# Kernel optimization log

Measured on AMD Instinct MI355X. Metric: run time of the kernel, lower is better.

## Reference

```python
import jax, jax.numpy as jnp
import numpy as np
from math import factorial

# ---- static sizes from S2ConvNet_original ----
B_IN, B1, B2 = 30, 10, 6   # bandwidths: input S2 grid, after conv1 (SO3), after conv2 (SO3)
F1, F2, FOUT = 20, 40, 10
BATCH = 128


def _wigner_d(l, beta):
    """Wigner small-d matrix d^l_{m',m}(beta); rows m'=-l..l, cols m=-l..l."""
    cb, sb = np.cos(beta / 2.0), np.sin(beta / 2.0)
    d = np.zeros((2 * l + 1, 2 * l + 1))
    for i, mp in enumerate(range(-l, l + 1)):
        for j, m in enumerate(range(-l, l + 1)):
            pref = np.sqrt(float(factorial(l + mp) * factorial(l - mp) * factorial(l + m) * factorial(l - m)))
            acc = 0.0
            for s in range(max(0, m - mp), min(l + m, l - mp) + 1):
                den = factorial(l + m - s) * factorial(s) * factorial(mp - m + s) * factorial(l - mp - s)
                acc += ((-1.0) ** (mp - m + s) / den) * cb ** (2 * l + m - mp - 2 * s) * sb ** (mp - m + 2 * s)
            d[i, j] = pref * acc
    return d


def _dh_quad(b):
    """Driscoll-Healy beta grid / weights: sum_j w_j g(beta_j) ~ int_0^pi g(b) sin(b) db."""
    j = np.arange(2 * b)
    beta = np.pi * (2 * j + 1) / (4 * b)
    k = np.arange(b)[:, None]
    w = (2.0 / b) * np.sin(beta) * np.sum(np.sin((2 * k + 1) * beta[None, :]) / (2 * k + 1), axis=0)
    return beta, w


def _s2_grid(max_beta=np.pi / 8, n_alpha=8, n_beta=3):
    beta = np.arange(1, n_beta + 1) * max_beta / n_beta
    alpha = np.linspace(0, 2 * np.pi, n_alpha, endpoint=False)
    Bm, Am = np.meshgrid(beta, alpha, indexing='ij')
    return np.stack([Bm.ravel(), Am.ravel()], 1)  # [24, 2]


def _so3_grid(max_beta=np.pi / 8, max_gamma=2 * np.pi, n_alpha=8, n_beta=3, n_gamma=8):
    beta = np.arange(1, n_beta + 1) * max_beta / n_beta
    alpha = np.linspace(0, 2 * np.pi, n_alpha, endpoint=False)
    pre_gamma = np.linspace(0, max_gamma, n_gamma, endpoint=False)
    Bm, Am, Cm = np.meshgrid(beta, alpha, pre_gamma, indexing='ij')
    return np.stack([Bm.ravel(), Am.ravel(), (Cm - Am).ravel()], 1)  # [192, 3]


# ---------- conv1: S2 analysis (b 30 -> 10) ----------
_beta30, _qw30 = _dh_quad(B_IN)
_A1 = np.concatenate(
    [np.stack([_wigner_d(l, bb)[:, l] for bb in _beta30])  # d^l_{m,0}(beta_j): [60, 2l+1]
     * (_qw30 * (2 * np.pi / (2 * B_IN)))[:, None]
     for l in range(B1)], axis=1)  # [60, 100]
_A1J = jnp.asarray(_A1.astype(np.float32))
_M1 = np.concatenate([np.arange(-l, l + 1) for l in range(B1)])
_M1_IDX = np.mod(_M1, 2 * B_IN)

_g1 = _s2_grid()
_Y1 = np.concatenate(
    [np.stack([_wigner_d(l, bb)[:, l] for bb in _g1[:, 0]])
     * np.exp(-1j * np.outer(_g1[:, 1], np.arange(-l, l + 1)))
     for l in range(B1)], axis=1)  # [24, 100] complex
_Y1J = jnp.asarray(_Y1.astype(np.complex64))
_SC1 = float(1.0 / np.sqrt(len(_g1) * 1 * (B1 ** 4) / (B_IN ** 2)))

# ---------- SO3 synthesis tables at b=10 ----------
_beta10, _qw10 = _dh_quad(B1)
_D1S = [jnp.asarray(((2 * l + 1) * np.stack([_wigner_d(l, bb) for bb in _beta10])).astype(np.float32)) for l in range(B1)]
_FM1 = [np.mod(np.arange(-l, l + 1), 2 * B1) for l in range(B1)]

# ---------- conv2: SO3 analysis (b 10 -> 6) ----------
_W3 = np.concatenate(
    [(np.stack([_wigner_d(l, bb) for bb in _beta10])  # [20, 2l+1, 2l+1]
      * (_qw10 * (2 * np.pi / (2 * B1)) ** 2)[:, None, None]).reshape(2 * B1, -1)
     for l in range(B2)], axis=1)  # [20, 286]
_W3J = jnp.asarray(_W3.astype(np.float32))
_M2 = np.concatenate([np.repeat(np.arange(-l, l + 1), 2 * l + 1) for l in range(B2)])
_N2 = np.concatenate([np.tile(np.arange(-l, l + 1), 2 * l + 1) for l in range(B2)])
_M2_IDX = np.mod(_M2, 2 * B1)
_N2_IDX = np.mod(_N2, 2 * B1)

_g2 = _so3_grid()
_Y2 = np.concatenate(
    [np.stack([_wigner_d(l, bb) for bb in _g2[:, 0]]).reshape(len(_g2), -1)
     * (np.exp(-1j * np.outer(_g2[:, 1], np.arange(-l, l + 1)))[:, :, None]
        * np.exp(-1j * np.outer(_g2[:, 2], np.arange(-l, l + 1)))[:, None, :]).reshape(len(_g2), -1)
     for l in range(B2)], axis=1)  # [192, 286] complex: D^l_{mn}(alpha,beta,gamma)
_Y2J = jnp.asarray(_Y2.astype(np.complex64))
_SC2 = float(1.0 / np.sqrt(len(_g2) * F1 * (B2 ** 3) / (B1 ** 3)))

# ---------- SO3 synthesis tables at b=6 + integration weights ----------
_beta6, _qw6 = _dh_quad(B2)
_D2S = [jnp.asarray(((2 * l + 1) * np.stack([_wigner_d(l, bb) for bb in _beta6])).astype(np.float32)) for l in range(B2)]
_FM2 = [np.mod(np.arange(-l, l + 1), 2 * B2) for l in range(B2)]
_W_INT = jnp.asarray((_qw6 * (2 * np.pi / (2 * B2)) ** 2).astype(np.float32))


def _forward(x, k1, bias1, k2, bias2, w_out, b_lin):
    Bn = x.shape[0]
    # ===== conv1: S2 correlation -> function on SO(3) at b=10 =====
    xf = jnp.fft.fft(x.astype(jnp.complex64), axis=-1)                 # FFT over alpha: [B,1,60,60]
    xhat = jnp.einsum('bfjs,js->sbf', xf[..., _M1_IDX], _A1J)          # [100,B,1] S2 spectrum
    k1h = jnp.einsum('iop,ps->sio', (k1 * _SC1).astype(jnp.complex64), _Y1J)  # [100,1,F1]
    Ffreq = jnp.zeros((Bn, F1, 2 * B1, 2 * B1, 2 * B1), jnp.complex64)  # [B,F1,beta,m,n]
    for l in range(B1):
        s0, s1 = l * l, (l + 1) * (l + 1)
        # z^l_{mn} = sum_fin xhat^l_m conj(khat^l_n)  (outer product per degree l)
        zl = jnp.einsum('mbi,nio->bmno', xhat[s0:s1], jnp.conj(k1h[s0:s1]))
        fb = jnp.einsum('bmno,jmn->bojmn', zl, _D1S[l])                # (2l+1) d^l_{mn}(beta_j)
        Ffreq = Ffreq.at[:, :, :, _FM1[l][:, None], _FM1[l][None, :]].add(fb)
    x1 = jnp.fft.ifft2(Ffreq, axes=(-2, -1)).real * float((2 * B1) ** 2)  # synth over alpha,gamma
    x1 = jax.nn.relu(x1 + bias1[None, :, None, None, None])            # [B,F1,20,20,20]
    # ===== conv2: SO(3) correlation -> b=6 =====
    x1f = jnp.fft.fft2(x1.astype(jnp.complex64), axes=(-2, -1))        # FFT over alpha,gamma
    xhat2 = jnp.einsum('bfjs,js->sbf', x1f[:, :, :, _M2_IDX, _N2_IDX], _W3J)  # [286,B,F1]
    k2h = jnp.einsum('iop,ps->sio', (k2 * _SC2).astype(jnp.complex64), _Y2J)  # [286,F1,F2]
    Ffreq2 = jnp.zeros((Bn, F2, 2 * B2, 2 * B2, 2 * B2), jnp.complex64)
    base = 0
    for l in range(B2):
        L = 2 * l + 1
        xl = xhat2[base:base + L * L].reshape(L, L, Bn, F1)            # [m,k,B,Fin]
        gl = jnp.conj(k2h[base:base + L * L].reshape(L, L, F1, F2))    # [n,k,Fin,Fout]
        zl = jnp.einsum('mkbi,nkio->bmno', xl, gl)                     # z^l = xhat^l ghat^l^H
        fb = jnp.einsum('bmno,jmn->bojmn', zl, _D2S[l])
        Ffreq2 = Ffreq2.at[:, :, :, _FM2[l][:, None], _FM2[l][None, :]].add(fb)
        base += L * L
    x2 = jnp.fft.ifft2(Ffreq2, axes=(-2, -1)).real * float((2 * B2) ** 2)
    x2 = jax.nn.relu(x2 + bias2[None, :, None, None, None])            # [B,F2,12,12,12]
    # ===== so3_integrate + linear head =====
    feat = jnp.einsum('bfjkp,j->bf', x2, _W_INT)                       # [B,F2]
    return feat @ w_out.T + b_lin


def setup_inputs() -> dict:
    key = jax.random.key(0)
    ks = jax.random.split(key, 4)
    return {
        'x': jax.random.normal(ks[0], (BATCH, 1, 2 * B_IN, 2 * B_IN), jnp.float32),
        'k1': jax.random.normal(ks[1], (1, F1, len(_g1)), jnp.float32),
        'bias1': jnp.zeros((F1,), jnp.float32),
        'k2': jax.random.normal(ks[2], (F1, F2, len(_g2)), jnp.float32),
        'bias2': jnp.zeros((F2,), jnp.float32),
        'w_out': jax.random.normal(ks[3], (FOUT, F2), jnp.float32) / np.sqrt(F2).astype(np.float32),
        'b_lin': jnp.zeros((FOUT,), jnp.float32),
    }


def reference(x, k1, bias1, k2, bias2, w_out, b_lin):
    return _forward(x, k1, bias1, k2, bias2, w_out, b_lin)
```

## Files before the change

### kernel.cpp

```cpp
#include <hip/hip_runtime.h>
#include <math.h>

#define PI_D 3.14159265358979323846

#define BATCH 128
#define F1 20
#define F2 40
#define FOUT 10
#define NS1 100
#define NS2 286
#define NH2 146

typedef float v2f __attribute__((ext_vector_type(2)));
#define PKFMA(a,b,c) __builtin_elementwise_fma((a),(b),(c))
#define SW(v) __builtin_shufflevector((v),(v),1,0)
static __device__ __forceinline__ v2f bc2(float s){ return (v2f){s,s}; }
static __device__ __forceinline__ v2f ldv(const float2* p){ return *(const v2f*)p; }

#define GLOAD_LDS16(g,l) __builtin_amdgcn_global_load_lds( \
  (const __attribute__((address_space(1))) void*)(g), \
  (__attribute__((address_space(3))) void*)(l), 16, 0, 0)

__constant__ int ZB10c[11] = {0,1,10,35,84,165,286,455,680,969,1330};
__constant__ int B2OFFc[7] = {0,1,10,35,84,165,286};
__constant__ int HOFFc[7]  = {0,1,6,19,44,85,146};
__constant__ float2 E8c[8] = {
  { 1.f, 0.f}, { 0.70710678118654752f,-0.70710678118654752f},
  { 0.f,-1.f}, {-0.70710678118654752f,-0.70710678118654752f},
  {-1.f, 0.f}, {-0.70710678118654752f, 0.70710678118654752f},
  { 0.f, 1.f}, { 0.70710678118654752f, 0.70710678118654752f}};

#define WFENCE do{ __builtin_amdgcn_sched_barrier(0); \
  asm volatile("s_waitcnt lgkmcnt(0)" ::: "memory"); \
  __builtin_amdgcn_sched_barrier(0); }while(0)

__device__ inline void h_decode(int h, int& l, int& m, int& n){
  l=0; while(HOFFc[l+1]<=h) ++l;
  int r=h-HOFFc[l], L=2*l+1;
  if(r<l+1){ n=0; m=r; }
  else { int q=r-(l+1); n=q/L+1; m=q%L-l; }
}

__device__ inline double ipow_d(double x, int n){ double r=1.0; for(int i=0;i<n;++i) r*=x; return r; }

__device__ double wigd_t(int l, int mp, int m, double beta, const double* F){
  double cb=cos(0.5*beta), sb=sin(0.5*beta);
  double pref=sqrt(F[l+mp]*F[l-mp]*F[l+m]*F[l-m]);
  int s0 = (m-mp>0) ? (m-mp) : 0;
  int s1 = (l+m < l-mp) ? (l+m) : (l-mp);
  double acc=0.0;
  for(int s=s0;s<=s1;++s){
    double den=F[l+m-s]*F[s]*F[mp-m+s]*F[l-mp-s];
    double t=ipow_d(cb,2*l+m-mp-2*s)*ipow_d(sb,mp-m+2*s)/den;
    acc += ((mp-m+s)&1)? -t : t;
  }
  return pref*acc;
}

__device__ double dhw(int b, int j){
  double beta=PI_D*(2*j+1)/(4.0*b);
  double s=0.0;
  for(int k=0;k<b;++k) s += sin((2*k+1)*beta)/(2*k+1);
  return (2.0/b)*sin(beta)*s;
}

__global__ void gen_all(const float* __restrict__ k2,
                        float* A1, float* D1SJ, float* W3H, float* D2SJ,
                        float* D3_2, float* D3_1, float* WINT,
                        float2* E60, float2* E20, float2* E12,
                        unsigned* zLUT, unsigned* xh2LUT, unsigned* h2LUT,
                        unsigned short* fhLUT, unsigned* aLUT,
                        float2* KA){
  __shared__ double factS[21];
  __shared__ double dhwS[60];
  __shared__ float2 E8L[8];
  int blk=blockIdx.x, t=threadIdx.x;
  if(t==0){ double f=1.0; factS[0]=1.0; for(int k=1;k<=20;++k){ f*=(double)k; factS[k]=f; } }
  if(blk<24){ if(t<60) dhwS[t]=dhw(30,t); }
  else if(blk>=76 && blk<82){ if(t<20) dhwS[t]=dhw(10,t); }
  if(t<8) E8L[t]=E8c[t];
  __syncthreads();
  const double* F=factS;
  if(blk<24){
    int idx=blk*256+t;
    if(idx<6000){
      int j=idx/NS1, s=idx%NS1;
      int l=0; while((l+1)*(l+1)<=s) ++l;
      int m=s-l*l-l;
      double beta=PI_D*(2*j+1)/120.0;
      A1[idx]=(float)(wigd_t(l,m,0,beta,F)*dhwS[j]*(2.0*PI_D/60.0));
    }
  } else if(blk<76){
    int idx=(blk-24)*256+t; if(idx>=13300) return;
    int j=idx/1330, s=idx%1330;
    int l=0; while(ZB10c[l+1]<=s) ++l;
    int r=s-ZB10c[l]; int L=2*l+1;
    int mi=r/L, ni=r%L;
    double beta=PI_D*(2*j+1)/40.0;
    float v=(float)((2*l+1)*wigd_t(l,mi-l,ni-l,beta,F));
    D1SJ[j*1330+s]=v;
    int s2=ZB10c[l]+(2*l-mi)*L+ni;
    D1SJ[(19-j)*1330+s2]=(ni&1)? -v : v;
  } else if(blk<82){
    int idx=(blk-76)*256+t;
    if(idx<10*NH2){
      int j=idx/NH2, h=idx%NH2;
      int l,m,n; h_decode(h,l,m,n);
      double beta=PI_D*(2*j+1)/40.0;
      double c=2.0*PI_D/20.0;
      float v=(float)(wigd_t(l,m,n,beta,F)*dhwS[j]*c*c);
      W3H[j*NH2+h]=v;
      if(n==0){
        W3H[(19-j)*NH2+h]=((l+m)&1)? -v : v;
      } else {
        int L=2*l+1;
        int hp=HOFFc[l]+(l+1)+(n-1)*L+(l-m);
        W3H[(19-j)*NH2+hp]=((l+n)&1)? -v : v;
      }
    }
  } else if(blk<89){
    int idx=(blk-82)*256+t; if(idx>=1716) return;
    int j=idx/286, s=idx%286;
    int l=0; while(B2OFFc[l+1]<=s) ++l;
    int r=s-B2OFFc[l]; int L=2*l+1;
    int mi=r/L, ni=r%L;
    double beta=PI_D*(2*j+1)/24.0;
    float v=(float)((2*l+1)*wigd_t(l,mi-l,ni-l,beta,F));
    D2SJ[j*286+s]=v;
    int s2=B2OFFc[l]+(2*l-mi)*L+ni;
    D2SJ[(11-j)*286+s2]=(ni&1)? -v : v;
  } else if(blk<93){
    int idx=(blk-89)*256+t; if(idx>=3*286) return;
    int bi=idx/286, s=idx%286;
    int l=0; while(B2OFFc[l+1]<=s) ++l;
    int r=s-B2OFFc[l]; int L=2*l+1;
    int mi=r/L, ni=r%L;
    double beta=(bi+1)*(PI_D/8.0)/3.0;
    D3_2[idx]=(float)wigd_t(l,mi-l,ni-l,beta,F);
  } else if(blk<95){
    int idx=(blk-93)*256+t; if(idx>=3*100) return;
    int bi=idx/100, s=idx%100;
    int l=0; while((l+1)*(l+1)<=s) ++l;
    int m=s-l*l-l;
    double beta=(bi+1)*(PI_D/8.0)/3.0;
    D3_1[idx]=(float)wigd_t(l,m,0,beta,F);
  } else if(blk==95){
    if(t<12){ double c=2.0*PI_D/12.0; WINT[t]=(float)(dhw(6,t)*c*c); }
    if(t<60){ double a=2.0*PI_D*t/60.0; E60[t]=make_float2((float)cos(a),(float)sin(a)); }
    if(t<20){ double a=2.0*PI_D*t/20.0; E20[t]=make_float2((float)cos(a),(float)sin(a)); }
    if(t<12){ double a=2.0*PI_D*t/12.0; E12[t]=make_float2((float)cos(a),(float)sin(a)); }
  } else if(blk<102){
    int idx=(blk-96)*256+t; if(idx>=1330) return;
    int l=0; while(ZB10c[l+1]<=idx) ++l;
    int r=idx-ZB10c[l], L=2*l+1;
    int mi=r/L, ni=r%L;
    unsigned s1x=(unsigned)(l*l+mi), s1k=(unsigned)(l*l+ni);
    zLUT[idx]=s1x|(s1k<<16);
  } else if(blk==102){
    if(t<146){
      int l,m,n; h_decode(t,l,m,n);
      int L=2*l+1;
      int s2 =B2OFFc[l]+(m+l)*L+(n+l);
      int s2p=B2OFFc[l]+(l-m)*L+(l-n);
      unsigned sg=(unsigned)((m+n)&1);
      xh2LUT[t]=(unsigned)s2 | ((unsigned)s2p<<10) | (sg<<20);
      h2LUT[t]=(unsigned)l | ((unsigned)(m+l)<<4) | ((unsigned)(n+l)<<8) | ((unsigned)s2<<12);
      fhLUT[t]=(unsigned short)((n==0)? m : 6+(n-1)*11+(m+5));
    }
  } else if(blk==103){
    if(t==0){
      int idx=0;
      for(int lm=0;lm<10;++lm){
        for(int m=0;m<10;++m){
          int nlo=(m==0)?0:-9;
          for(int n=nlo;n<10;++n){
            int an=n<0?-n:n;
            int lmin=m>an?m:an;
            if(lmin!=lm) continue;
            int L=2*lm+1;
            int zi=ZB10c[lm]+(m+lm)*L+(n+lm);
            aLUT[idx++]=(unsigned)zi | ((unsigned)m<<11) | ((unsigned)(n+9)<<15) | ((unsigned)lm<<20);
          }
        }
      }
    }
  } else {
    int idx=(blk-104)*256+t;
    if(idx<153600){
      int ai=idx&7, q=(idx>>3)&7;
      int r2=idx>>6;
      int bi=r2%3, io=r2/3;
      const float* kp=k2+(size_t)io*192+bi*64+ai*8;
      v2f acc={0.f,0.f};
      int ph=0;
      #pragma unroll
      for(int gi=0;gi<8;++gi){
        acc=PKFMA(bc2(kp[gi]), ldv(&E8L[ph]), acc);
        ph=(ph+q)&7;
      }
      KA[(size_t)io*192+bi*64+q*8+ai]=make_float2(acc.x,acc.y);
    }
  }
}

__global__ __launch_bounds__(256) void front_k(const float* __restrict__ x,
    const float* __restrict__ k1,
    const float2* __restrict__ E60, const float* __restrict__ A1,
    const float* __restrict__ D3_1,
    float2* __restrict__ XHAT, float2* __restrict__ K1H){
  int blk=blockIdx.x, t=threadIdx.x;
  if(blk<128){
    __shared__ __align__(16) float xs[3600];
    __shared__ float2 E60s[60];
    __shared__ float2 XFs[1140];
    if(t<60){ float2 e=E60[t]; E60s[t]=make_float2(e.x,-e.y); }
    {
      const float4* src=(const float4*)(x+blk*3600);
      float4* dst=(float4*)xs;
      for(int i=t;i<900;i+=256) GLOAD_LDS16(src+i, dst+(i&~63));
    }
    __syncthreads();
    for(int idx=t; idx<1140; idx+=256){
      int j=idx/19, mi=idx%19;
      int step=(mi<9)? mi+51 : mi-9;
      bool modd = ((mi&1)==0);
      const float* xr=xs+j*60;
      v2f acc={0.f,0.f};
      int k=0;
      for(int a=0;a<30;++a){
        float xv = modd ? (xr[a]-xr[a+30]) : (xr[a]+xr[a+30]);
        acc=PKFMA(bc2(xv), ldv(&E60s[k]), acc);
        k+=step; if(k>=60)k-=60;
      }
      XFs[idx]=make_float2(acc.x,acc.y);
    }
    __syncthreads();
    for(int s=t; s<100; s+=256){
      int l=0; while((l+1)*(l+1)<=s) ++l;
      int m=s-l*l-l;
      const float2* xf=&XFs[m+9];
      v2f acc={0.f,0.f};
      for(int j=0;j<60;++j){
        acc=PKFMA(bc2(A1[j*NS1+s]), ldv(&xf[j*19]), acc);
      }
      XHAT[blk*NS1+s]=make_float2(acc.x,acc.y);
    }
  } else {
    __shared__ float2 E8s[8];
    if(t<8) E8s[t]=E8c[t];
    __syncthreads();
    int idx=(blk-128)*256+t;
    if(idx<F1*NS1){
      int o=idx/NS1, s=idx%NS1;
      int l=0; while((l+1)*(l+1)<=s) ++l;
      int m=s-l*l-l;
      int mm=m&7;
      v2f acc={0.f,0.f};
      for(int bi=0;bi<3;++bi){
        v2f sum={0.f,0.f};
        int q=0;
        #pragma unroll
        for(int ai=0;ai<8;++ai){
          sum=PKFMA(bc2(k1[o*24+bi*8+ai]), ldv(&E8s[q]), sum);
          q=(q+mm)&7;
        }
        acc=PKFMA(bc2(D3_1[bi*100+s]), sum, acc);
      }
      const float SC1f = 0.06123724356957945f;
      K1H[idx]=make_float2(acc.x*SC1f, acc.y*SC1f);
    }
  }
}

__global__ __launch_bounds__(512,6) void fused1(
    const float2* __restrict__ XHAT, const float2* __restrict__ K1H,
    const float* __restrict__ D1SJ, const float* __restrict__ W3H,
    const float2* __restrict__ E20, const float* __restrict__ bias1,
    const unsigned* __restrict__ zLUT, const unsigned* __restrict__ xh2LUT,
    const unsigned short* __restrict__ fhLUT, const unsigned* __restrict__ aLUT,
    float2* __restrict__ XH2){
  const int b=blockIdx.x, o=blockIdx.y, t=threadIdx.x;
  const int ln=t&63, w=t>>6;
  __shared__ __align__(16) float2 zS[1330];
  __shared__ __align__(16) float2 TWE2[400];
  __shared__ __align__(16) float2 regA[8][200];
  __shared__ __align__(16) float2 regB[8][190];

  for(int idx=t; idx<400; idx+=512){
    int r=idx/20, c=idx%20;
    TWE2[idx]=E20[(r*c)%20];
  }
  {
    float2* st=regA[0];
    if(t<100) st[t]=XHAT[b*NS1+t];
    else if(t<200) st[t]=K1H[o*NS1+(t-100)];
  }
  __syncthreads();
  {
    const float2* st=regA[0];
    for(int idx=t; idx<1330; idx+=512){
      unsigned u=zLUT[idx];
      v2f xa=ldv(&st[u&0xffff]);
      v2f kb=ldv(&st[100+(u>>16)]);
      v2f p1=xa*kb, p2=xa*SW(kb);
      zS[idx]=make_float2(p1.x+p1.y, p2.y-p2.x);
    }
  }
  __syncthreads();

  const float bb1=bias1[o];
  float2* G  = regA[w];
  float*  vbF= (float*)regA[w];
  float2* Fq = regA[w];
  float*  RB = (float*)regB[w];
  float*  Sx = RB;
  float*  Sy = RB+180;
  float*  T0f= RB+360;
  float2* U_T= regB[w];
  v2f fa0={0.f,0.f}, fa1=fa0, fa2=fa0;

  const int BROW[19]={11,12,13,14,15,16,17,18,19,0,1,2,3,4,5,6,7,8,9};

  for(int jq=0;jq<3;++jq){
    const int j=jq*8+w;
    const bool act=(j<20);
    const float* Dg=D1SJ + (act? j*1330 : 0);
    if(act) for(int idx=ln; idx<181; idx+=64){
      unsigned au=aLUT[idx];
      int zi=au&2047;
      int m=(au>>11)&15, n9=(au>>15)&31, l=(au>>20)&15;
      int L=2*l+1;
      int m2=2*m+2;
      v2f a0={0.f,0.f};
      for(; l<10; ++l){
        a0=PKFMA(ldv(&zS[zi]), bc2(Dg[zi]), a0);
        zi += L*L + 2*L + m2; L += 2;
      }
      *(v2f*)&G[m*19+n9]=a0;
    }
    WFENCE;
    if(act){
    if(ln<45){
      int mb=ln/5+1, gp=(ln%5)*2;
      const float2* Gr=&G[mb*19];
      v2f E1a={0.f,0.f},E2a=E1a,O1a=E1a,O2a=E1a;
      v2f E1b=E1a,E2b=E1a,O1b=E1a,O2b=E1a;
      #pragma unroll
      for(int c=0;c<19;++c){
        v2f gv=ldv(&Gr[c]);
        const float* er=(const float*)&TWE2[BROW[c]*20+gp];
        float4 e01=*(const float4*)er;
        v2f e0={e01.x,e01.y}, e1={e01.z,e01.w};
        if(c&1){
          E1a=PKFMA(gv,e0,E1a); E2a=PKFMA(gv,SW(e0),E2a);
          E1b=PKFMA(gv,e1,E1b); E2b=PKFMA(gv,SW(e1),E2b);
        } else {
          O1a=PKFMA(gv,e0,O1a); O2a=PKFMA(gv,SW(e0),O2a);
          O1b=PKFMA(gv,e1,O1b); O2b=PKFMA(gv,SW(e1),O2b);
        }
      }
      int si=(mb-1)*20+gp;
      float exa=E1a.x-E1a.y, oxa=O1a.x-O1a.y;
      float eya=E2a.x+E2a.y, oya=O2a.x+O2a.y;
      float exb=E1b.x-E1b.y, oxb=O1b.x-O1b.y;
      float eyb=E2b.x+E2b.y, oyb=O2b.x+O2b.y;
      *(v2f*)&Sx[si]   =(v2f){2.f*(exa+oxa), 2.f*(exb+oxb)};
      *(v2f*)&Sx[si+10]=(v2f){2.f*(exa-oxa), 2.f*(exb-oxb)};
      *(v2f*)&Sy[si]   =(v2f){2.f*(eya+oya), 2.f*(eyb+oyb)};
      *(v2f*)&Sy[si+10]=(v2f){2.f*(eya-oya), 2.f*(eyb-oyb)};
    } else if(ln<50){
      int gt=(ln-45)*2;
      float g0x=G[9].x;
      float Ea=0.f,Eb=0.f,Oa=0.f,Ob=0.f;
      #pragma unroll
      for(int n=1;n<10;++n){
        float2 gv=G[9+n];
        const float* er=(const float*)&TWE2[n*20+gt];
        float4 e01=*(const float4*)er;
        float ra=gv.x*e01.x-gv.y*e01.y;
        float rb=gv.x*e01.z-gv.y*e01.w;
        if((n&1)==0){ Ea+=ra; Eb+=rb; } else { Oa+=ra; Ob+=rb; }
      }
      T0f[gt]   =g0x+2.f*(Ea+Oa);
      T0f[gt+1] =g0x+2.f*(Eb+Ob);
      T0f[gt+10]=g0x+2.f*(Ea-Oa);
      T0f[gt+11]=g0x+2.f*(Eb-Ob);
    }
    }
    WFENCE;
    if(act && ln<50){
      int a=ln/5, g0=(ln%5)*4;
      v2f i01={T0f[g0]+bb1, T0f[g0+1]+bb1};
      v2f i23={T0f[g0+2]+bb1, T0f[g0+3]+bb1};
      v2f P01={0.f,0.f},P23=P01,Q01=P01,Q23=P01;
      #pragma unroll
      for(int m=1;m<10;++m){
        float2 e=TWE2[a*20+m];
        v2f sx01=*(const v2f*)&Sx[(m-1)*20+g0];
        v2f sx23=*(const v2f*)&Sx[(m-1)*20+g0+2];
        v2f sy01=*(const v2f*)&Sy[(m-1)*20+g0];
        v2f sy23=*(const v2f*)&Sy[(m-1)*20+g0+2];
        if(m&1){
          Q01=PKFMA(bc2(e.x),sx01,Q01); Q01=PKFMA(bc2(-e.y),sy01,Q01);
          Q23=PKFMA(bc2(e.x),sx23,Q23); Q23=PKFMA(bc2(-e.y),sy23,Q23);
        } else {
          P01=PKFMA(bc2(e.x),sx01,P01); P01=PKFMA(bc2(-e.y),sy01,P01);
          P23=PKFMA(bc2(e.x),sx23,P23); P23=PKFMA(bc2(-e.y),sy23,P23);
        }
      }
      v2f z2={0.f,0.f};
      v2f vA01=i01+P01+Q01, vA23=i23+P23+Q23;
      v2f vB01=i01+P01-Q01, vB23=i23+P23-Q23;
      *(v2f*)&vbF[a*20+g0]       =__builtin_elementwise_max(vA01,z2);
      *(v2f*)&vbF[a*20+g0+2]     =__builtin_elementwise_max(vA23,z2);
      *(v2f*)&vbF[(a+10)*20+g0]  =__builtin_elementwise_max(vB01,z2);
      *(v2f*)&vbF[(a+10)*20+g0+2]=__builtin_elementwise_max(vB23,z2);
    }
    WFENCE;
    if(act && ln<60){
      int a=ln/3, np=ln%3;
      int nu0=2*np, nu1=2*np+1;
      int r0=(np==0)?0:(20-2*np);
      int r1=19-2*np;
      const float* vp=&vbF[a*20];
      const float2* T0r=&TWE2[r0*20];
      const float2* T1r=&TWE2[r1*20];
      v2f u0={0.f,0.f}, u1=u0;
      #pragma unroll
      for(int g=0;g<10;++g){
        float va=vp[g], vb=vp[g+10];
        u0=PKFMA(bc2(va+vb), ldv(&T0r[g]), u0);
        u1=PKFMA(bc2(va-vb), ldv(&T1r[g]), u1);
      }
      *(v2f*)&U_T[nu0*20+a]=u0; *(v2f*)&U_T[nu1*20+a]=u1;
    }
    WFENCE;
    if(act && ln<61){
      int mu,nu;
      if(ln<6){ mu=ln; nu=0; } else { int q=ln-6; nu=q/11+1; mu=q%11-5; }
      int mm=(mu+20)%20;
      int rm=(20-mm)%20;
      bool modd=(mm&1);
      const float2* Ur=&U_T[nu*20];
      const float2* Er=&TWE2[rm*20];
      v2f p1={0.f,0.f}, p2=p1;
      #pragma unroll
      for(int a=0;a<10;++a){
        v2f ua=ldv(&Ur[a]), ub=ldv(&Ur[a+10]);
        v2f u = modd ? (ua-ub) : (ua+ub);
        v2f e=ldv(&Er[a]);
        p1=PKFMA(u,e,p1);
        p2=PKFMA(u,SW(e),p2);
      }
      Fq[ln]=make_float2(p1.x-p1.y, p2.x+p2.y);
    }
    WFENCE;
    if(act){
      const float* W3r=W3H + j*NH2;
      fa0=PKFMA(bc2(W3r[ln]),    ldv(&Fq[fhLUT[ln]]),    fa0);
      fa1=PKFMA(bc2(W3r[64+ln]), ldv(&Fq[fhLUT[64+ln]]), fa1);
      if(ln<18) fa2=PKFMA(bc2(W3r[128+ln]), ldv(&Fq[fhLUT[128+ln]]), fa2);
    }
    WFENCE;
  }
  regB[w][ln]=make_float2(fa0.x,fa0.y);
  regB[w][64+ln]=make_float2(fa1.x,fa1.y);
  if(ln<18) regB[w][128+ln]=make_float2(fa2.x,fa2.y);
  __syncthreads();
  float2* XHrow=XH2+(size_t)(b*F1+o)*286;
  for(int h=t; h<146; h+=512){
    unsigned u=xh2LUT[h];
    int s2=u&1023, s2p=(u>>10)&1023;
    float sg=((u>>20)&1)? -1.f : 1.f;
    float2 a0=regB[0][h], a1=regB[1][h], a2=regB[2][h], a3=regB[3][h];
    float2 a4=regB[4][h], a5=regB[5][h], a6=regB[6][h], a7=regB[7][h];
    float2 a=make_float2(a0.x+a1.x+a2.x+a3.x+a4.x+a5.x+a6.x+a7.x,
                         a0.y+a1.y+a2.y+a3.y+a4.y+a5.y+a6.y+a7.y);
    XHrow[s2 ]=a;
    XHrow[s2p]=make_float2(sg*a.x, -sg*a.y);
  }
}

__global__ __launch_bounds__(192) void k2h_k(const float2* __restrict__ KA,
                      const float* __restrict__ D3_2,
                      const unsigned* __restrict__ h2LUT, const unsigned* __restrict__ xh2LUT,
                      float2* __restrict__ K2H){
  __shared__ float2 kaS[192];
  __shared__ float2 E8s[8];
  int io=blockIdx.x, t=threadIdx.x;
  int i=io/F2, o=io%F2;
  if(t<8) E8s[t]=E8c[t];
  kaS[t]=KA[(size_t)io*192+t];
  __syncthreads();
  if(t>=146) return;
  unsigned hu=h2LUT[t];
  int l=hu&15, mi=(hu>>4)&15, ni=(hu>>8)&15, s2=hu>>12;
  int m=mi-l, n=ni-l;
  unsigned xu=xh2LUT[t];
  int s2p=(xu>>10)&1023;
  float sg=((xu>>20)&1)? -1.f : 1.f;
  int q=n&7, p=(m-n)&7;
  v2f a1={0.f,0.f}, a2=a1;
  for(int bi=0;bi<3;++bi){
    const float2* kp=&kaS[bi*64+q*8];
    v2f s1={0.f,0.f}, s2v=s1;
    int ph=0;
    #pragma unroll
    for(int ai=0;ai<8;++ai){
      v2f ka=ldv(&kp[ai]), e=ldv(&E8s[ph]);
      s1=PKFMA(ka,e,s1); s2v=PKFMA(ka,SW(e),s2v);
      ph=(ph+p)&7;
    }
    v2f dv=bc2(D3_2[bi*286+s2]);
    a1=PKFMA(dv,s1,a1); a2=PKFMA(dv,s2v,a2);
  }
  const float SC2f = 0.034722222222222224f;
  float re=(a1.x-a1.y)*SC2f, im=(a2.x+a2.y)*SC2f;
  float2* Krow=K2H+(size_t)(o*F1+i)*286;
  Krow[s2 ]=make_float2(re,im);
  Krow[s2p]=make_float2(sg*re,-sg*im);
}

__global__ __launch_bounds__(256,3) void fused2(
    const float2* __restrict__ XH2, const float2* __restrict__ K2H,
    const float* __restrict__ D2SJ, const float* __restrict__ WINT,
    const float2* __restrict__ E12, const float* __restrict__ bias2,
    const unsigned* __restrict__ h2LUT, const unsigned* __restrict__ xh2LUT,
    float* __restrict__ FEAT){
  const int b=blockIdx.x, o=blockIdx.y, t=threadIdx.x;
  const int ln=t&63, w=t>>6;
  __shared__ __align__(16) float2 Xs[2541];
  __shared__ __align__(16) float2 Ks[2541];
  __shared__ float2 zpS[1144];
  __shared__ float2 z2S[286];
  __shared__ float  redS[256];
  float2* alias=(float2*)Xs;
  float2* TWE12=alias;

  const int gb[4]={0,84,165,286};
  const int hb[4]={0,44,85,146};
  for(int grp=0; grp<3; ++grp){
    int row0=gb[grp], rows=gb[grp+1]-row0;
    {
      int cnt=20*rows;
      const float2* xbase=XH2+(size_t)b*F1*286+row0;
      const float2* kbase=K2H+(size_t)o*F1*286+row0;
      for(int idx=t; idx<cnt; idx+=256){
        int i=idx/rows, sl=idx-i*rows;
        Xs[sl*21+i]=xbase[i*286+sl];
        Ks[sl*21+i]=kbase[i*286+sl];
      }
    }
    __syncthreads();
    int nh=hb[grp+1]-hb[grp];
    for(int idx=t; idx<4*nh; idx+=256){
      int hl=idx>>2, iq=idx&3;
      int h=hb[grp]+hl;
      unsigned hu=h2LUT[h];
      int l=hu&15, mi=(hu>>4)&15, ni=(hu>>8)&15, s2=hu>>12;
      int L=2*l+1;
      int xr0=(B2OFFc[l]-row0)+mi*L;
      int kr0=(B2OFFc[l]-row0)+ni*L;
      v2f p1={0.f,0.f}, p2=p1;
      for(int k=0;k<L;++k){
        const float2* xp=Xs+(xr0+k)*21+iq*5;
        const float2* kp=Ks+(kr0+k)*21+iq*5;
        #pragma unroll
        for(int i=0;i<5;++i){
          v2f xa=ldv(&xp[i]), kb=ldv(&kp[i]);
          p1=PKFMA(xa,kb,p1);
          p2=PKFMA(xa,SW(kb),p2);
        }
      }
      zpS[iq*286+s2]=make_float2(p1.x+p1.y, p2.y-p2.x);
    }
    __syncthreads();
  }
  for(int idx=t; idx<146; idx+=256){
    unsigned xu=xh2LUT[idx];
    int s2=xu&1023, s2p=(xu>>10)&1023;
    float sg=((xu>>20)&1)? -1.f : 1.f;
    float2 a;
    a.x=zpS[0*286+s2].x+zpS[1*286+s2].x+zpS[2*286+s2].x+zpS[3*286+s2].x;
    a.y=zpS[0*286+s2].y+zpS[1*286+s2].y+zpS[2*286+s2].y+zpS[3*286+s2].y;
    z2S[s2]=a;
    z2S[s2p]=make_float2(sg*a.x,-sg*a.y);
  }
  __syncthreads();
  for(int idx=t; idx<144; idx+=256){
    int r=idx/12, c=idx%12;
    TWE12[idx]=E12[(r*c)%12];
  }
  __syncthreads();

  float2* base2=alias+144+w*400;
  float2* G2_0=base2; float2* G2_1=base2+66; float2* G2_2=base2+132;
  float*  SP=(float*)(base2+198);
  float*  S2x0=SP, *S2x1=SP+60, *S2x2=SP+120;
  float*  S2y0=SP+180, *S2y1=SP+240, *S2y2=SP+300;
  float*  T02=SP+360;
  float personal=0.f;
  const float b2v=bias2[o];
  const int j0=3*w, j1=3*w+1, j2=3*w+2;
  const float* Dg0=D2SJ + j0*286;
  const float* Dg1=D2SJ + j1*286;
  const float* Dg2=D2SJ + j2*286;
  const int BR12[11]={7,8,9,10,11,0,1,2,3,4,5};

  if(ln<61){
    int m,n;
    if(ln<6){m=0;n=ln;} else {int qq=ln-6;m=qq/11+1;n=qq%11-5;}
    int an=n<0?-n:n; int l=m>an?m:an; int L=2*l+1;
    int zi=B2OFFc[l]+(m+l)*L+(n+l); int m2=2*m+2;
    v2f a0={0.f,0.f}, a1=a0, a2=a0;
    for(;l<6;++l){
      v2f zv=ldv(&z2S[zi]);
      a0=PKFMA(zv, bc2(Dg0[zi]), a0);
      a1=PKFMA(zv, bc2(Dg1[zi]), a1);
      a2=PKFMA(zv, bc2(Dg2[zi]), a2);
      zi+=L*L+2*L+m2; L+=2;
    }
    int gi=m*11+(n+5);
    *(v2f*)&G2_0[gi]=a0; *(v2f*)&G2_1[gi]=a1; *(v2f*)&G2_2[gi]=a2;
  }
  WFENCE;
  if(ln<30){
    int m=ln/6+1, g=ln%6;
    v2f E1_0={0.f,0.f},E2_0=E1_0,O1_0=E1_0,O2_0=E1_0;
    v2f E1_1=E1_0,E2_1=E1_0,O1_1=E1_0,O2_1=E1_0;
    v2f E1_2=E1_0,E2_2=E1_0,O1_2=E1_0,O2_2=E1_0;
    #pragma unroll
    for(int c=0;c<11;++c){
      float2 ef=TWE12[BR12[c]*12+g];
      v2f e={ef.x,ef.y};
      v2f g0=ldv(&G2_0[m*11+c]), g1=ldv(&G2_1[m*11+c]), g2=ldv(&G2_2[m*11+c]);
      if(c&1){
        E1_0=PKFMA(g0,e,E1_0); E2_0=PKFMA(g0,SW(e),E2_0);
        E1_1=PKFMA(g1,e,E1_1); E2_1=PKFMA(g1,SW(e),E2_1);
        E1_2=PKFMA(g2,e,E1_2); E2_2=PKFMA(g2,SW(e),E2_2);
      } else {
        O1_0=PKFMA(g0,e,O1_0); O2_0=PKFMA(g0,SW(e),O2_0);
        O1_1=PKFMA(g1,e,O1_1); O2_1=PKFMA(g1,SW(e),O2_1);
        O1_2=PKFMA(g2,e,O1_2); O2_2=PKFMA(g2,SW(e),O2_2);
      }
    }
    int si=(m-1)*12+g;
    {
      float Ex=E1_0.x-E1_0.y, Ox=O1_0.x-O1_0.y;
      float Ey=E2_0.x+E2_0.y, Oy=O2_0.x+O2_0.y;
      S2x0[si]=2.f*(Ex+Ox); S2x0[si+6]=2.f*(Ex-Ox);
      S2y0[si]=2.f*(Ey+Oy); S2y0[si+6]=2.f*(Ey-Oy);
    }
    {
      float Ex=E1_1.x-E1_1.y, Ox=O1_1.x-O1_1.y;
      float Ey=E2_1.x+E2_1.y, Oy=O2_1.x+O2_1.y;
      S2x1[si]=2.f*(Ex+Ox); S2x1[si+6]=2.f*(Ex-Ox);
      S2y1[si]=2.f*(Ey+Oy); S2y1[si+6]=2.f*(Ey-Oy);
    }
    {
      float Ex=E1_2.x-E1_2.y, Ox=O1_2.x-O1_2.y;
      float Ey=E2_2.x+E2_2.y, Oy=O2_2.x+O2_2.y;
      S2x2[si]=2.f*(Ex+Ox); S2x2[si+6]=2.f*(Ex-Ox);
      S2y2[si]=2.f*(Ey+Oy); S2y2[si+6]=2.f*(Ey-Oy);
    }
  } else if(ln<42){
    int g=ln-30;
    float r0=G2_0[5].x, r1=G2_1[5].x, r2=G2_2[5].x;
    #pragma unroll
    for(int n=1;n<6;++n){
      float2 e=TWE12[n*12+g];
      float2 g0=G2_0[5+n], g1=G2_1[5+n], g2=G2_2[5+n];
      r0+=2.f*(g0.x*e.x-g0.y*e.y);
      r1+=2.f*(g1.x*e.x-g1.y*e.y);
      r2+=2.f*(g2.x*e.x-g2.y*e.y);
    }
    T02[g]=r0; T02[12+g]=r1; T02[24+g]=r2;
  }
  WFENCE;
  if(ln<36){
    float w0=WINT[j0], w1=WINT[j1], w2=WINT[j2];
    int a=ln/3, g4=(ln%3)*4;
    v2f iA0={T02[g4]+b2v, T02[g4+1]+b2v},       iB0={T02[g4+2]+b2v, T02[g4+3]+b2v};
    v2f iA1={T02[12+g4]+b2v, T02[12+g4+1]+b2v}, iB1={T02[12+g4+2]+b2v, T02[12+g4+3]+b2v};
    v2f iA2={T02[24+g4]+b2v, T02[24+g4+1]+b2v}, iB2={T02[24+g4+2]+b2v, T02[24+g4+3]+b2v};
    #pragma unroll
    for(int m=1;m<6;++m){
      float2 e=TWE12[a*12+m];
      v2f ex=bc2(e.x), eny=bc2(-e.y);
      int si=(m-1)*12+g4;
      v2f sx, sy;
      sx=*(const v2f*)&S2x0[si];   sy=*(const v2f*)&S2y0[si];
      iA0=PKFMA(ex,sx,iA0); iA0=PKFMA(eny,sy,iA0);
      sx=*(const v2f*)&S2x0[si+2]; sy=*(const v2f*)&S2y0[si+2];
      iB0=PKFMA(ex,sx,iB0); iB0=PKFMA(eny,sy,iB0);
      sx=*(const v2f*)&S2x1[si];   sy=*(const v2f*)&S2y1[si];
      iA1=PKFMA(ex,sx,iA1); iA1=PKFMA(eny,sy,iA1);
      sx=*(const v2f*)&S2x1[si+2]; sy=*(const v2f*)&S2y1[si+2];
      iB1=PKFMA(ex,sx,iB1); iB1=PKFMA(eny,sy,iB1);
      sx=*(const v2f*)&S2x2[si];   sy=*(const v2f*)&S2y2[si];
      iA2=PKFMA(ex,sx,iA2); iA2=PKFMA(eny,sy,iA2);
      sx=*(const v2f*)&S2x2[si+2]; sy=*(const v2f*)&S2y2[si+2];
      iB2=PKFMA(ex,sx,iB2); iB2=PKFMA(eny,sy,iB2);
    }
    v2f z2={0.f,0.f};
    v2f rA0=__builtin_elementwise_max(iA0,z2), rB0=__builtin_elementwise_max(iB0,z2);
    v2f rA1=__builtin_elementwise_max(iA1,z2), rB1=__builtin_elementwise_max(iB1,z2);
    v2f rA2=__builtin_elementwise_max(iA2,z2), rB2=__builtin_elementwise_max(iB2,z2);
    personal += w0*(rA0.x+rA0.y+rB0.x+rB0.y)
              + w1*(rA1.x+rA1.y+rB1.x+rB1.y)
              + w2*(rA2.x+rA2.y+rB2.x+rB2.y);
  }
  redS[t]=personal;
  __syncthreads();
  for(int s=128;s>0;s>>=1){
    if(t<s) redS[t]+=redS[t+s];
    __syncthreads();
  }
  if(t==0) FEAT[b*F2+o]=redS[0];
}

__global__ void head_k(const float* __restrict__ FEAT, const float* __restrict__ w_out,
                       const float* __restrict__ b_lin, float* __restrict__ out){
  int idx=blockIdx.x*blockDim.x+threadIdx.x;
  if(idx>=BATCH*FOUT) return;
  int b=idx/FOUT, q=idx%FOUT;
  float acc=b_lin[q];
  for(int f=0;f<F2;++f) acc += FEAT[b*F2+f]*w_out[q*F2+f];
  out[idx]=acc;
}

extern "C" void kernel_launch(void* const* d_in, const int* in_sizes, int n_in,
                              void* d_out, int out_size, void* d_ws, size_t ws_size,
                              hipStream_t stream) {
  const float* x    =(const float*)d_in[0];
  const float* k1   =(const float*)d_in[1];
  const float* bias1=(const float*)d_in[2];
  const float* k2   =(const float*)d_in[3];
  const float* bias2=(const float*)d_in[4];
  const float* w_out=(const float*)d_in[5];
  const float* b_lin=(const float*)d_in[6];
  float* out=(float*)d_out;

  char* ws=(char*)d_ws;
  float*  A1   =(float* )(ws+0);
  float*  D1SJ =(float* )(ws+24000);
  float*  W3H  =(float* )(ws+130400);
  float*  D2SJ =(float* )(ws+142080);
  float*  D3_2 =(float* )(ws+155808);
  float*  D3_1 =(float* )(ws+159248);
  float*  WINT =(float* )(ws+160448);
  float2* E60  =(float2*)(ws+160496);
  float2* E20  =(float2*)(ws+160976);
  float2* E12  =(float2*)(ws+161136);
  unsigned* zLUT=(unsigned*)(ws+161248);
  unsigned* xh2LUT=(unsigned*)(ws+166576);
  unsigned* h2LUT =(unsigned*)(ws+167160);
  unsigned short* fhLUT=(unsigned short*)(ws+167744);
  unsigned* aLUT =(unsigned*)(ws+168048);
  float2* XHAT =(float2*)(ws+168784);
  float2* K1H  =(float2*)(ws+271184);
  float2* KA   =(float2*)(ws+287184);
  float2* XH2  =(float2*)(ws+1515984);
  float2* K2H  =(float2*)(ws+7373264);
  float*  FEAT =(float* )(ws+9203664);

  (void)in_sizes; (void)n_in; (void)out_size; (void)ws_size;

  gen_all<<<704,256,0,stream>>>(k2,A1,D1SJ,W3H,D2SJ,D3_2,D3_1,WINT,E60,E20,E12,
                                zLUT,xh2LUT,h2LUT,fhLUT,aLUT,KA);
  front_k<<<136,256,0,stream>>>(x,k1,E60,A1,D3_1,XHAT,K1H);
  dim3 g1(BATCH,F1);
  fused1<<<g1,512,0,stream>>>(XHAT,K1H,D1SJ,W3H,E20,bias1,zLUT,xh2LUT,fhLUT,aLUT,XH2);
  k2h_k<<<F1*F2,192,0,stream>>>(KA,D3_2,h2LUT,xh2LUT,K2H);
  dim3 g2(BATCH,F2);
  fused2<<<g2,256,0,stream>>>(XH2,K2H,D2SJ,WINT,E12,bias2,h2LUT,xh2LUT,FEAT);
  head_k<<<(BATCH*FOUT+255)/256,256,0,stream>>>(FEAT,w_out,b_lin,out);
}
```

Measured before the change: 237.2 us.

## Stage conv2 inputs with async global-to-LDS copies in two channel halves

The second-layer fused kernel no longer copies X and K spectra into shared memory with scalar, transposed stores across three row groups. It now copies contiguous halves of ten input channels with 16-byte global_load_lds transfers. In the compute loop each thread owns a full output coefficient and loops over ten channels in a channel-major layout. This cuts the staging passes from three to two, removes the per-element index arithmetic and makes the global reads coalesced. In exchange, only 146 of 256 threads work in the contraction phase, the padded layout that avoided bank conflicts is gone, and the reduction buffer now reuses zpS, which needs an extra barrier.

Result: no change. 241.4 us (+1.8%).

```diff
diff --git a/kernel.cpp b/kernel.cpp
--- a/kernel.cpp
+++ b/kernel.cpp
@@ -529,60 +529,52 @@
     float* __restrict__ FEAT){
   const int b=blockIdx.x, o=blockIdx.y, t=threadIdx.x;
   const int ln=t&63, w=t>>6;
-  __shared__ __align__(16) float2 Xs[2541];
-  __shared__ __align__(16) float2 Ks[2541];
-  __shared__ float2 zpS[1144];
+  __shared__ __align__(16) float2 Xs[2860];
+  __shared__ __align__(16) float2 Ks[2860];
+  __shared__ float2 zpS[572];
   __shared__ float2 z2S[286];
-  __shared__ float  redS[256];
+  float* redS=(float*)zpS;
   float2* alias=(float2*)Xs;
   float2* TWE12=alias;
 
-  const int gb[4]={0,84,165,286};
-  const int hb[4]={0,44,85,146};
-  for(int grp=0; grp<3; ++grp){
-    int row0=gb[grp], rows=gb[grp+1]-row0;
+  for(int hf=0; hf<2; ++hf){
     {
-      int cnt=20*rows;
-      const float2* xbase=XH2+(size_t)b*F1*286+row0;
-      const float2* kbase=K2H+(size_t)o*F1*286+row0;
-      for(int idx=t; idx<cnt; idx+=256){
-        int i=idx/rows, sl=idx-i*rows;
-        Xs[sl*21+i]=xbase[i*286+sl];
-        Ks[sl*21+i]=kbase[i*286+sl];
+      const float4* xsrc=(const float4*)(XH2+(size_t)(b*F1+hf*10)*286);
+      const float4* ksrc=(const float4*)(K2H+(size_t)(o*F1+hf*10)*286);
+      float4* xd=(float4*)Xs; float4* kd=(float4*)Ks;
+      for(int i4=t;i4<1430;i4+=256){
+        int wb=i4&~63;
+        GLOAD_LDS16(xsrc+i4, xd+wb);
+        GLOAD_LDS16(ksrc+i4, kd+wb);
       }
     }
     __syncthreads();
-    int nh=hb[grp+1]-hb[grp];
-    for(int idx=t; idx<4*nh; idx+=256){
-      int hl=idx>>2, iq=idx&3;
-      int h=hb[grp]+hl;
+    for(int h=t; h<146; h+=256){
       unsigned hu=h2LUT[h];
       int l=hu&15, mi=(hu>>4)&15, ni=(hu>>8)&15, s2=hu>>12;
       int L=2*l+1;
-      int xr0=(B2OFFc[l]-row0)+mi*L;
-      int kr0=(B2OFFc[l]-row0)+ni*L;
+      int xr0=B2OFFc[l]+mi*L;
+      int kr0=B2OFFc[l]+ni*L;
       v2f p1={0.f,0.f}, p2=p1;
-      for(int k=0;k<L;++k){
-        const float2* xp=Xs+(xr0+k)*21+iq*5;
-        const float2* kp=Ks+(kr0+k)*21+iq*5;
-        #pragma unroll
-        for(int i=0;i<5;++i){
-          v2f xa=ldv(&xp[i]), kb=ldv(&kp[i]);
+      for(int i=0;i<10;++i){
+        const float2* xp=Xs+i*286+xr0;
+        const float2* kp=Ks+i*286+kr0;
+        for(int k=0;k<L;++k){
+          v2f xa=ldv(&xp[k]), kb=ldv(&kp[k]);
           p1=PKFMA(xa,kb,p1);
           p2=PKFMA(xa,SW(kb),p2);
         }
       }
-      zpS[iq*286+s2]=make_float2(p1.x+p1.y, p2.y-p2.x);
+      zpS[hf*286+h]=make_float2(p1.x+p1.y, p2.y-p2.x);
     }
     __syncthreads();
   }
-  for(int idx=t; idx<146; idx+=256){
-    unsigned xu=xh2LUT[idx];
+  for(int h=t; h<146; h+=256){
+    unsigned xu=xh2LUT[h];
     int s2=xu&1023, s2p=(xu>>10)&1023;
     float sg=((xu>>20)&1)? -1.f : 1.f;
-    float2 a;
-    a.x=zpS[0*286+s2].x+zpS[1*286+s2].x+zpS[2*286+s2].x+zpS[3*286+s2].x;
-    a.y=zpS[0*286+s2].y+zpS[1*286+s2].y+zpS[2*286+s2].y+zpS[3*286+s2].y;
+    float2 pa=zpS[h], pb=zpS[286+h];
+    float2 a=make_float2(pa.x+pb.x, pa.y+pb.y);
     z2S[s2]=a;
     z2S[s2p]=make_float2(sg*a.x,-sg*a.y);
   }
@@ -710,6 +702,7 @@
               + w1*(rA1.x+rA1.y+rB1.x+rB1.y)
               + w2*(rA2.x+rA2.y+rB2.x+rB2.y);
   }
+  __syncthreads();
   redS[t]=personal;
   __syncthreads();
   for(int s=128;s>0;s>>=1){
```
